# Optimization experiments

Measured on AMD Instinct MI355X. Metric: run time of the kernel, lower is better.

## Reference

```python
import jax, jax.numpy as jnp
import numpy as np

V, T, E, H, B, S = 50000, 45, 256, 512, 32, 256


def setup_inputs() -> dict:
    key = jax.random.key(0)
    ks = jax.random.split(key, 14)
    s = 0.05
    return dict(
        x=jax.random.randint(ks[0], (B, S), 0, V),
        tags=jax.random.randint(ks[1], (B, S), 0, T),
        mask=jnp.ones((B, S), dtype=bool),
        emb=jax.random.normal(ks[2], (V, E), jnp.float32),
        Wih_f=jax.random.normal(ks[3], (4 * H, E), jnp.float32) * s,
        Whh_f=jax.random.normal(ks[4], (4 * H, H), jnp.float32) * s,
        bih_f=jnp.zeros((4 * H,), jnp.float32),
        bhh_f=jnp.zeros((4 * H,), jnp.float32),
        Wih_b=jax.random.normal(ks[5], (4 * H, E), jnp.float32) * s,
        Whh_b=jax.random.normal(ks[6], (4 * H, H), jnp.float32) * s,
        bih_b=jnp.zeros((4 * H,), jnp.float32),
        bhh_b=jnp.zeros((4 * H,), jnp.float32),
        Wout=jax.random.normal(ks[7], (T, 2 * H), jnp.float32) * s,
        bout=jnp.zeros((T,), jnp.float32),
        start=jax.random.normal(ks[8], (T,), jnp.float32) * 0.1,
        end=jax.random.normal(ks[9], (T,), jnp.float32) * 0.1,
        trans=jax.random.normal(ks[10], (T, T), jnp.float32) * 0.1,
    )


def _lstm_dir(xp, Whh, reverse):
    # xp: [S, B, 4H] precomputed input projection + biases; gate order i,f,g,o (torch)
    Bn = xp.shape[1]
    Hn = Whh.shape[1]
    def step(carry, g_in):
        h, c = carry
        g = g_in + h @ Whh.T
        i, f, gg, o = jnp.split(g, 4, axis=-1)
        c = jax.nn.sigmoid(f) * c + jax.nn.sigmoid(i) * jnp.tanh(gg)
        h = jax.nn.sigmoid(o) * jnp.tanh(c)
        return (h, c), h
    init = (jnp.zeros((Bn, Hn), xp.dtype), jnp.zeros((Bn, Hn), xp.dtype))
    _, hs = jax.lax.scan(step, init, xp, reverse=reverse)
    return hs  # [S, B, H]


def _crf_nll(emissions, tags, mask, start, end, trans):
    # emissions: [B, S, T]; neg mean log-likelihood (torchcrf, reduction='mean')
    mf = mask.astype(emissions.dtype)
    em_tag = jnp.take_along_axis(emissions, tags[:, :, None], axis=2)[:, :, 0]  # [B,S]
    num = start[tags[:, 0]] + em_tag[:, 0]
    num = num + ((trans[tags[:, :-1], tags[:, 1:]] + em_tag[:, 1:]) * mf[:, 1:]).sum(1)
    seq_ends = mf.sum(1).astype(tags.dtype) - 1
    last_tags = jnp.take_along_axis(tags, seq_ends[:, None], axis=1)[:, 0]
    num = num + end[last_tags]
    def denom_step(alpha, inp):
        em_t, m_t = inp  # [B,T], [B]
        nxt = jax.nn.logsumexp(alpha[:, :, None] + trans[None, :, :] + em_t[:, None, :], axis=1)
        return jnp.where(m_t[:, None] > 0, nxt, alpha), None
    alpha0 = start[None, :] + emissions[:, 0]
    em_rest = emissions.transpose(1, 0, 2)[1:]  # [S-1, B, T]
    alpha, _ = jax.lax.scan(denom_step, alpha0, (em_rest, mf.T[1:]))
    logZ = jax.nn.logsumexp(alpha + end[None, :], axis=1)
    return -(num - logZ).mean()


def reference(x, tags, mask, emb, Wih_f, Whh_f, bih_f, bhh_f,
              Wih_b, Whh_b, bih_b, bhh_b, Wout, bout, start, end, trans):
    embeds = emb[x]                      # [B, S, E]
    xs = embeds.transpose(1, 0, 2)       # [S, B, E]
    xp_f = jnp.einsum('sbe,ge->sbg', xs, Wih_f) + bih_f + bhh_f
    hs_f = _lstm_dir(xp_f, Whh_f, False)
    xp_b = jnp.einsum('sbe,ge->sbg', xs, Wih_b) + bih_b + bhh_b
    hs_b = _lstm_dir(xp_b, Whh_b, True)
    hcat = jnp.concatenate([hs_f, hs_b], axis=-1)          # [S, B, 2H]
    emissions = jnp.einsum('sbh,th->sbt', hcat, Wout) + bout
    emissions = emissions.transpose(1, 0, 2)                # [B, S, T]
    return _crf_nll(emissions, tags, mask, start, end, trans)
```

## Files before the change

kernel.cpp:

```cpp
#include <hip/hip_runtime.h>
#include <stdint.h>

#define S_LEN 256
#define B_N 32
#define H_N 512
#define E_N 256
#define T_N 45
#define G4H 2048

typedef unsigned short u16;
typedef unsigned int u32;
typedef u16 u16x8 __attribute__((ext_vector_type(8)));
typedef u16 u16x4 __attribute__((ext_vector_type(4)));
typedef u32 u32x4 __attribute__((ext_vector_type(4)));
typedef __bf16 bf16x8 __attribute__((ext_vector_type(8)));
typedef float f32x4 __attribute__((ext_vector_type(4)));
typedef unsigned long long u64;

#define OFF_FLG   0ull
#define OFF_ATOK  256ull
#define OFF_WIHF  (OFF_ATOK + 4194304ull)
#define OFF_WIHB  (OFF_WIHF + 1048576ull)
#define OFF_WHHF  (OFF_WIHB + 1048576ull)
#define OFF_WHHB  (OFF_WHHF + 2097152ull)
#define OFF_WOUT  (OFF_WHHB + 2097152ull)
#define OFF_BSF   (OFF_WOUT + 98304ull)
#define OFF_BSB   (OFF_BSF + 8192ull)
#define OFF_XPF   (OFF_BSB + 8192ull)
#define OFF_XPB   (OFF_XPF + 33554432ull)
#define OFF_HSF   (OFF_XPB + 33554432ull)
#define OFF_HSB   (OFF_HSF + 8421376ull)
#define OFF_EM    (OFF_HSB + 8421376ull)
#define OFF_VAL   (OFF_EM + 1572864ull)

__device__ __forceinline__ u16 f2bf(float f) {
  union { float f; unsigned u; } v; v.f = f;
  unsigned r = v.u + 0x7FFFu + ((v.u >> 16) & 1u);
  return (u16)(r >> 16);
}
__device__ __forceinline__ float bf2f(u16 b) {
  union { unsigned u; float f; } v; v.u = ((unsigned)b) << 16;
  return v.f;
}
__device__ __forceinline__ bf16x8 ld8(const u16* p) {
  u16x8 v = *reinterpret_cast<const u16x8*>(p);
  return __builtin_bit_cast(bf16x8, v);
}
__device__ __forceinline__ void st_h8cc(u16* p, u16x4 v) {
  __hip_atomic_store(reinterpret_cast<u64*>(p), __builtin_bit_cast(u64, v),
                     __ATOMIC_RELAXED, __HIP_MEMORY_SCOPE_AGENT);
}
__device__ __forceinline__ u32x4 ld16cc(const u16* p) {
  u32x4 r;
  asm volatile("global_load_dwordx4 %0, %1, off sc0 sc1"
               : "=v"(r) : "v"(p) : "memory");
  return r;
}
__device__ __forceinline__ f32x4 mfma16(bf16x8 a, bf16x8 b, f32x4 c) {
  return __builtin_amdgcn_mfma_f32_16x16x32_bf16(a, b, c, 0, 0, 0);
}
__device__ __forceinline__ float sigm(float x) { return 1.f / (1.f + __expf(-x)); }
__device__ __forceinline__ float tanhf_(float x) {
  float ax = fabsf(x);
  float e = __expf(-2.f * ax);
  float t = 1.f - 2.f * e / (1.f + e);
  return (x < 0.f) ? -t : t;
}
__device__ __forceinline__ float wredmax(float v) {
  #pragma unroll
  for (int m = 1; m < 64; m <<= 1) v = fmaxf(v, __shfl_xor(v, m));
  return v;
}
__device__ __forceinline__ float wredsum(float v) {
  #pragma unroll
  for (int m = 1; m < 64; m <<= 1) v += __shfl_xor(v, m);
  return v;
}

__global__ void k_castA(const int* __restrict__ x, const float* __restrict__ emb,
                        u16* __restrict__ atok) {
  int idx = blockIdx.x * 256 + threadIdx.x;
  int t = idx >> 5;
  int e0 = (idx & 31) << 3;
  int s = t >> 5, b = t & 31;
  int xid = x[b * S_LEN + s];
  const float4* p = reinterpret_cast<const float4*>(emb + (size_t)xid * E_N + e0);
  float4 lo = p[0], hi = p[1];
  u16x8 o;
  o[0] = f2bf(lo.x); o[1] = f2bf(lo.y); o[2] = f2bf(lo.z); o[3] = f2bf(lo.w);
  o[4] = f2bf(hi.x); o[5] = f2bf(hi.y); o[6] = f2bf(hi.z); o[7] = f2bf(hi.w);
  *reinterpret_cast<u16x8*>(atok + (size_t)t * E_N + e0) = o;
}

__global__ void k_castW(const float* __restrict__ WihF, const float* __restrict__ WihB,
                        const float* __restrict__ WhhF, const float* __restrict__ WhhB,
                        const float* __restrict__ Wout,
                        const float* __restrict__ bihF, const float* __restrict__ bhhF,
                        const float* __restrict__ bihB, const float* __restrict__ bhhB,
                        u16* wihf, u16* wihb, u16* whhf, u16* whhb, u16* woutp,
                        float* bsf, float* bsb, u16* hsf, u16* hsb) {
  int i = blockIdx.x * 256 + threadIdx.x;
  if (i < 524288) { wihf[i] = f2bf(WihF[i]); return; }
  i -= 524288;
  if (i < 524288) { wihb[i] = f2bf(WihB[i]); return; }
  i -= 524288;
  if (i < 1048576) { whhf[i] = f2bf(WhhF[i]); return; }
  i -= 1048576;
  if (i < 1048576) { whhb[i] = f2bf(WhhB[i]); return; }
  i -= 1048576;
  if (i < 49152) {
    int n = i >> 10, k = i & 1023;
    woutp[i] = (n < T_N) ? f2bf(Wout[n * 1024 + k]) : (u16)0;
    return;
  }
  i -= 49152;
  if (i < 2048) { bsf[i] = bihF[i] + bhhF[i]; return; }
  i -= 2048;
  if (i < 2048) { bsb[i] = bihB[i] + bhhB[i]; return; }
  i -= 2048;
  if (i < 16384) { hsf[i] = 0; return; }
  i -= 16384;
  if (i < 16384) { hsb[(size_t)256 * 16384 + i] = 0; return; }
}

__global__ __launch_bounds__(256) void k_gemm_xp(
    const u16* __restrict__ atok, const u16* __restrict__ wihF, const u16* __restrict__ wihB,
    const float* __restrict__ bsF, const float* __restrict__ bsB,
    u16* __restrict__ xpF, u16* __restrict__ xpB) {
  int wid = blockIdx.x;
  int dir = wid >> 10, rem = wid & 1023;
  const int wave = threadIdx.x >> 6, lane = threadIdx.x & 63;
  const int lr = lane & 15, lh = lane >> 4;
  const int t0 = (rem >> 3) * 64;
  const int g0 = (rem & 7) * 256 + wave * 64;
  const u16* wih = dir ? wihB : wihF;
  const float* bs = dir ? bsB : bsF;
  u16* xp = dir ? xpB : xpF;
  f32x4 acc[4][4] = {};
  for (int kk = 0; kk < 8; ++kk) {
    int e = kk * 32 + lh * 8;
    bf16x8 a[4], bfr[4];
    #pragma unroll
    for (int mi = 0; mi < 4; ++mi) a[mi] = ld8(atok + (size_t)(t0 + 16 * mi + lr) * E_N + e);
    #pragma unroll
    for (int ni = 0; ni < 4; ++ni) bfr[ni] = ld8(wih + (size_t)(g0 + 16 * ni + lr) * E_N + e);
    #pragma unroll
    for (int mi = 0; mi < 4; ++mi)
      #pragma unroll
      for (int ni = 0; ni < 4; ++ni) acc[mi][ni] = mfma16(a[mi], bfr[ni], acc[mi][ni]);
  }
  #pragma unroll
  for (int ni = 0; ni < 4; ++ni) {
    int g = g0 + 16 * ni + lr;
    float bsv = bs[g];
    #pragma unroll
    for (int mi = 0; mi < 4; ++mi)
      #pragma unroll
      for (int r = 0; r < 4; ++r) {
        int t = t0 + 16 * mi + 4 * lh + r;
        xp[(size_t)t * G4H + g] = f2bf(acc[mi][ni][r] + bsv);
      }
  }
}

__global__ __launch_bounds__(128, 1) void k_lstm(
    const u16* __restrict__ whhF, const u16* __restrict__ whhB,
    const u16* __restrict__ xpF, const u16* __restrict__ xpB,
    u16* __restrict__ hsF, u16* __restrict__ hsB, int* flags) {
  const int dir = blockIdx.x >> 5;
  const int w = blockIdx.x & 31;
  const int nt = threadIdx.x >> 6;
  const int lane = threadIdx.x & 63;
  const int lr = lane & 15, lh = lane >> 4;
  const u16* whh = dir ? whhB : whhF;
  const u16* xp = dir ? xpB : xpF;
  u16* hs = dir ? hsB : hsF;
  int* flg = flags + dir * 32;

  bf16x8 A[4][16];
  #pragma unroll
  for (int mt = 0; mt < 4; ++mt) {
    const u16* base = whh + (size_t)(mt * 512 + 16 * w + lr) * H_N + lh * 8;
    #pragma unroll
    for (int kk = 0; kk < 16; ++kk) A[mt][kk] = ld8(base + kk * 32);
  }
  const int b = nt * 16 + lr;
  const int j0 = 16 * w + 4 * lh;
  const int fidx = lane & 31;
  float cst[4] = {0.f, 0.f, 0.f, 0.f};

  for (int t = 0; t < S_LEN; ++t) {
    const int s = dir ? (S_LEN - 1 - t) : t;
    const int slot_r = dir ? (s + 1) : s;
    const int slot_w = dir ? s : (s + 1);
    u16x4 xq[4];
    const u16* xpt = xp + ((size_t)(s * B_N + b)) * G4H + j0;
    #pragma unroll
    for (int mt = 0; mt < 4; ++mt) xq[mt] = *reinterpret_cast<const u16x4*>(xpt + mt * 512);

    const u16* hp = hs + ((size_t)slot_r * B_N + b) * H_N + lh * 8;
    u32x4 raw[16];
    #pragma unroll
    for (int kk = 0; kk < 16; ++kk) raw[kk] = ld16cc(hp + kk * 32);
    asm volatile("s_waitcnt vmcnt(0)" ::: "memory");
    __builtin_amdgcn_sched_barrier(0);
    u32 bad = 0;
    #pragma unroll
    for (int kk = 0; kk < 16; ++kk) {
      #pragma unroll
      for (int d = 0; d < 4; ++d) bad |= (raw[kk][d] == 0xFFFFFFFFu) ? 1u : 0u;
    }
    if (!__all(bad == 0)) {
      for (;;) {
        int f = __hip_atomic_load(&flg[fidx], __ATOMIC_RELAXED, __HIP_MEMORY_SCOPE_AGENT);
        if (__all(f >= t)) break;
        __builtin_amdgcn_s_sleep(1);
      }
      #pragma unroll
      for (int kk = 0; kk < 16; ++kk) raw[kk] = ld16cc(hp + kk * 32);
      asm volatile("s_waitcnt vmcnt(0)" ::: "memory");
      __builtin_amdgcn_sched_barrier(0);
    }

    f32x4 acc[4] = {};
    #pragma unroll
    for (int kk = 0; kk < 16; ++kk) {
      bf16x8 Bf = __builtin_bit_cast(bf16x8, raw[kk]);
      #pragma unroll
      for (int mt = 0; mt < 4; ++mt) acc[mt] = mfma16(A[mt][kk], Bf, acc[mt]);
    }
    u16x4 hv;
    #pragma unroll
    for (int r = 0; r < 4; ++r) {
      float gi = acc[0][r] + bf2f(xq[0][r]);
      float gf = acc[1][r] + bf2f(xq[1][r]);
      float gg = acc[2][r] + bf2f(xq[2][r]);
      float go = acc[3][r] + bf2f(xq[3][r]);
      float c = sigm(gf) * cst[r] + sigm(gi) * tanhf_(gg);
      cst[r] = c;
      hv[r] = f2bf(sigm(go) * tanhf_(c));
    }
    st_h8cc(hs + ((size_t)slot_w * B_N + b) * H_N + j0, hv);
    asm volatile("s_waitcnt vmcnt(0)" ::: "memory");
    __syncthreads();
    if (threadIdx.x == 0)
      __hip_atomic_store(&flg[w], t + 1, __ATOMIC_RELAXED, __HIP_MEMORY_SCOPE_AGENT);
  }
}

__global__ __launch_bounds__(256) void k_gemm_em(
    const u16* __restrict__ hsF, const u16* __restrict__ hsB,
    const u16* __restrict__ woutp, const float* __restrict__ bout, float* __restrict__ em) {
  const int wave = threadIdx.x >> 6, lane = threadIdx.x & 63;
  const int lr = lane & 15, lh = lane >> 4;
  const int t0 = blockIdx.x * 64 + wave * 16;
  f32x4 acc[3] = {};
  for (int kk = 0; kk < 32; ++kk) {
    int k = kk * 32 + lh * 8;
    int t = t0 + lr;
    int s = t >> 5, bt = t & 31;
    const u16* ap = (kk < 16) ? (hsF + ((size_t)(s + 1) * B_N + bt) * H_N + k)
                              : (hsB + ((size_t)s * B_N + bt) * H_N + (k - 512));
    bf16x8 a = ld8(ap);
    #pragma unroll
    for (int ni = 0; ni < 3; ++ni) {
      bf16x8 bb = ld8(woutp + (size_t)(16 * ni + lr) * 1024 + k);
      acc[ni] = mfma16(a, bb, acc[ni]);
    }
  }
  #pragma unroll
  for (int ni = 0; ni < 3; ++ni) {
    int tag = 16 * ni + lr;
    float bo = (tag < T_N) ? bout[tag] : 0.f;
    #pragma unroll
    for (int r = 0; r < 4; ++r) {
      int t = t0 + 4 * lh + r;
      em[(size_t)t * 48 + tag] = acc[ni][r] + bo;
    }
  }
}

__global__ __launch_bounds__(256) void k_crf(
    const float* __restrict__ em, const int* __restrict__ tags,
    const float* __restrict__ start, const float* __restrict__ endv,
    const float* __restrict__ trans, float* __restrict__ val) {
  __shared__ float tl[T_N * T_N];
  __shared__ float al[64];
  __shared__ float part[4][64];
  const int b = blockIdx.x;
  const int tid = threadIdx.x, wq = tid >> 6, lane = tid & 63;
  for (int i = tid; i < T_N * T_N; i += 256) tl[i] = trans[i];
  __syncthreads();
  float acur = (lane < T_N) ? (start[lane] + em[(size_t)b * 48 + lane]) : -1e30f;
  float shift = wredmax(acur);
  if (wq == 0) al[lane] = acur;
  __syncthreads();
  const int tbeg = wq * 12;
  const int tend = (tbeg + 12 < T_N) ? (tbeg + 12) : T_N;
  for (int s = 1; s < S_LEN; ++s) {
    float sm = 0.f;
    if (lane < T_N) {
      for (int t = tbeg; t < tend; ++t)
        sm += __expf(al[t] + tl[t * T_N + lane] - shift);
    }
    part[wq][lane] = sm;
    __syncthreads();
    float tot = part[0][lane] + part[1][lane] + part[2][lane] + part[3][lane];
    float anew = -1e30f;
    if (lane < T_N) anew = shift + __logf(tot) + em[((size_t)s * B_N + b) * 48 + lane];
    acur = anew;
    shift = wredmax(acur);
    __syncthreads();
    if (wq == 0) al[lane] = acur;
    __syncthreads();
  }
  float z = (lane < T_N) ? (acur + endv[lane]) : -1e30f;
  float m = wredmax(z);
  float sum = wredsum((lane < T_N) ? __expf(z - m) : 0.f);
  float logZ = m + __logf(sum);
  if (wq == 0) {
    float np = 0.f;
    #pragma unroll
    for (int q = 0; q < 4; ++q) {
      int s = 1 + lane * 4 + q;
      if (s < S_LEN) {
        int tp = tags[b * S_LEN + s - 1], tc = tags[b * S_LEN + s];
        np += tl[tp * T_N + tc] + em[((size_t)s * B_N + b) * 48 + tc];
      }
    }
    np = wredsum(np);
    if (lane == 0) {
      int tg0 = tags[b * S_LEN], tgL = tags[b * S_LEN + S_LEN - 1];
      float num = start[tg0] + em[(size_t)b * 48 + tg0] + np + endv[tgL];
      val[b] = num - logZ;
    }
  }
}

__global__ void k_final(const float* __restrict__ val, float* __restrict__ out) {
  int lane = threadIdx.x & 63;
  float v = (lane < B_N) ? val[lane] : 0.f;
  v = wredsum(v);
  if (threadIdx.x == 0) out[0] = -(v / (float)B_N);
}

extern "C" void kernel_launch(void* const* d_in, const int* in_sizes, int n_in,
                              void* d_out, int out_size, void* d_ws, size_t ws_size,
                              hipStream_t stream) {
  const int* x = (const int*)d_in[0];
  const int* tags = (const int*)d_in[1];
  const float* emb = (const float*)d_in[3];
  const float* WihF = (const float*)d_in[4];
  const float* WhhF = (const float*)d_in[5];
  const float* bihF = (const float*)d_in[6];
  const float* bhhF = (const float*)d_in[7];
  const float* WihB = (const float*)d_in[8];
  const float* WhhB = (const float*)d_in[9];
  const float* bihB = (const float*)d_in[10];
  const float* bhhB = (const float*)d_in[11];
  const float* Wout = (const float*)d_in[12];
  const float* bout = (const float*)d_in[13];
  const float* start = (const float*)d_in[14];
  const float* endv = (const float*)d_in[15];
  const float* trans = (const float*)d_in[16];
  float* out = (float*)d_out;
  char* ws = (char*)d_ws;

  u16* atok = (u16*)(ws + OFF_ATOK);
  u16* wihf = (u16*)(ws + OFF_WIHF);
  u16* wihb = (u16*)(ws + OFF_WIHB);
  u16* whhf = (u16*)(ws + OFF_WHHF);
  u16* whhb = (u16*)(ws + OFF_WHHB);
  u16* woutp = (u16*)(ws + OFF_WOUT);
  float* bsf = (float*)(ws + OFF_BSF);
  float* bsb = (float*)(ws + OFF_BSB);
  u16* xpf = (u16*)(ws + OFF_XPF);
  u16* xpb = (u16*)(ws + OFF_XPB);
  u16* hsf = (u16*)(ws + OFF_HSF);
  u16* hsb = (u16*)(ws + OFF_HSB);
  float* emis = (float*)(ws + OFF_EM);
  float* val = (float*)(ws + OFF_VAL);

  hipMemsetAsync(ws + OFF_FLG, 0, 256, stream);
  hipMemsetAsync(ws + OFF_HSF + 32768ull, 0xFF, 8388608ull, stream);
  hipMemsetAsync(ws + OFF_HSB, 0xFF, 8388608ull, stream);
  k_castA<<<1024, 256, 0, stream>>>(x, emb, atok);
  k_castW<<<12624, 256, 0, stream>>>(WihF, WihB, WhhF, WhhB, Wout, bihF, bhhF, bihB, bhhB,
                                     wihf, wihb, whhf, whhb, woutp, bsf, bsb, hsf, hsb);
  k_gemm_xp<<<2048, 256, 0, stream>>>(atok, wihf, wihb, bsf, bsb, xpf, xpb);
  k_lstm<<<64, 128, 0, stream>>>(whhf, whhb, xpf, xpb, hsf, hsb, (int*)(ws + OFF_FLG));
  k_gemm_em<<<128, 256, 0, stream>>>(hsf, hsb, woutp, bout, emis);
  k_crf<<<32, 256, 0, stream>>>(emis, tags, start, endv, trans, val);
  k_final<<<1, 64, 0, stream>>>(val, out);
}
```

Baseline: 1.527 ms.

## Switch LSTM to per-wave flag sync and single-wave shuffle-based CRF

The LSTM recurrence drops its speculative sentinel-value check (0xFF-filled h buffers plus a reload on a miss). Instead, each wave polls 64 per-wave flags before loading h, and the block-wide __syncthreads is gone because each wave publishes its own flag. This also removes the two 8MB memsets of the h buffers. The CRF forward pass moves from four waves with shared-memory partial sums and three barriers per step to one wave using shuffles and three independent accumulators. The trade-off is that every step now pays a flag-polling round trip even when data is already ready.

```diff
diff --git a/kernel.cpp b/kernel.cpp
--- a/kernel.cpp
+++ b/kernel.cpp
@@ -18,7 +18,7 @@
 typedef unsigned long long u64;
 
 #define OFF_FLG   0ull
-#define OFF_ATOK  256ull
+#define OFF_ATOK  1024ull
 #define OFF_WIHF  (OFF_ATOK + 4194304ull)
 #define OFF_WIHB  (OFF_WIHF + 1048576ull)
 #define OFF_WHHF  (OFF_WIHB + 1048576ull)
@@ -175,7 +175,8 @@
   const u16* whh = dir ? whhB : whhF;
   const u16* xp = dir ? xpB : xpF;
   u16* hs = dir ? hsB : hsF;
-  int* flg = flags + dir * 32;
+  int* flg = flags + dir * 64;
+  const int myf = w * 2 + nt;
 
   bf16x8 A[4][16];
   #pragma unroll
@@ -186,7 +187,6 @@
   }
   const int b = nt * 16 + lr;
   const int j0 = 16 * w + 4 * lh;
-  const int fidx = lane & 31;
   float cst[4] = {0.f, 0.f, 0.f, 0.f};
 
   for (int t = 0; t < S_LEN; ++t) {
@@ -198,29 +198,20 @@
     #pragma unroll
     for (int mt = 0; mt < 4; ++mt) xq[mt] = *reinterpret_cast<const u16x4*>(xpt + mt * 512);
 
+    if (t > 0) {
+      for (;;) {
+        int f = __hip_atomic_load(&flg[lane], __ATOMIC_RELAXED, __HIP_MEMORY_SCOPE_AGENT);
+        if (__all(f >= t)) break;
+        __builtin_amdgcn_s_sleep(1);
+      }
+    }
+
     const u16* hp = hs + ((size_t)slot_r * B_N + b) * H_N + lh * 8;
     u32x4 raw[16];
     #pragma unroll
     for (int kk = 0; kk < 16; ++kk) raw[kk] = ld16cc(hp + kk * 32);
     asm volatile("s_waitcnt vmcnt(0)" ::: "memory");
     __builtin_amdgcn_sched_barrier(0);
-    u32 bad = 0;
-    #pragma unroll
-    for (int kk = 0; kk < 16; ++kk) {
-      #pragma unroll
-      for (int d = 0; d < 4; ++d) bad |= (raw[kk][d] == 0xFFFFFFFFu) ? 1u : 0u;
-    }
-    if (!__all(bad == 0)) {
-      for (;;) {
-        int f = __hip_atomic_load(&flg[fidx], __ATOMIC_RELAXED, __HIP_MEMORY_SCOPE_AGENT);
-        if (__all(f >= t)) break;
-        __builtin_amdgcn_s_sleep(1);
-      }
-      #pragma unroll
-      for (int kk = 0; kk < 16; ++kk) raw[kk] = ld16cc(hp + kk * 32);
-      asm volatile("s_waitcnt vmcnt(0)" ::: "memory");
-      __builtin_amdgcn_sched_barrier(0);
-    }
 
     f32x4 acc[4] = {};
     #pragma unroll
@@ -242,9 +233,8 @@
     }
     st_h8cc(hs + ((size_t)slot_w * B_N + b) * H_N + j0, hv);
     asm volatile("s_waitcnt vmcnt(0)" ::: "memory");
-    __syncthreads();
-    if (threadIdx.x == 0)
-      __hip_atomic_store(&flg[w], t + 1, __ATOMIC_RELAXED, __HIP_MEMORY_SCOPE_AGENT);
+    if (lane == 0)
+      __hip_atomic_store(&flg[myf], t + 1, __ATOMIC_RELAXED, __HIP_MEMORY_SCOPE_AGENT);
   }
 }
 
@@ -280,60 +270,47 @@
   }
 }
 
-__global__ __launch_bounds__(256) void k_crf(
+__global__ __launch_bounds__(64) void k_crf(
     const float* __restrict__ em, const int* __restrict__ tags,
     const float* __restrict__ start, const float* __restrict__ endv,
     const float* __restrict__ trans, float* __restrict__ val) {
-  __shared__ float tl[T_N * T_N];
-  __shared__ float al[64];
-  __shared__ float part[4][64];
+  __shared__ float tl[T_N * T_N + 32];
   const int b = blockIdx.x;
-  const int tid = threadIdx.x, wq = tid >> 6, lane = tid & 63;
-  for (int i = tid; i < T_N * T_N; i += 256) tl[i] = trans[i];
+  const int lane = threadIdx.x;
+  for (int i = lane; i < T_N * T_N + 32; i += 64)
+    tl[i] = (i < T_N * T_N) ? trans[i] : 0.f;
   __syncthreads();
   float acur = (lane < T_N) ? (start[lane] + em[(size_t)b * 48 + lane]) : -1e30f;
-  float shift = wredmax(acur);
-  if (wq == 0) al[lane] = acur;
-  __syncthreads();
-  const int tbeg = wq * 12;
-  const int tend = (tbeg + 12 < T_N) ? (tbeg + 12) : T_N;
   for (int s = 1; s < S_LEN; ++s) {
-    float sm = 0.f;
-    if (lane < T_N) {
-      for (int t = tbeg; t < tend; ++t)
-        sm += __expf(al[t] + tl[t * T_N + lane] - shift);
-    }
-    part[wq][lane] = sm;
-    __syncthreads();
-    float tot = part[0][lane] + part[1][lane] + part[2][lane] + part[3][lane];
-    float anew = -1e30f;
-    if (lane < T_N) anew = shift + __logf(tot) + em[((size_t)s * B_N + b) * 48 + lane];
-    acur = anew;
-    shift = wredmax(acur);
-    __syncthreads();
-    if (wq == 0) al[lane] = acur;
-    __syncthreads();
+    float shift = wredmax(acur);
+    float emv = (lane < 48) ? em[((size_t)s * B_N + b) * 48 + lane] : 0.f;
+    float s0 = 0.f, s1 = 0.f, s2 = 0.f;
+    #pragma unroll
+    for (int t = 0; t < T_N; t += 3) {
+      s0 += __expf(__shfl(acur, t)     + tl[t * T_N + lane]       - shift);
+      s1 += __expf(__shfl(acur, t + 1) + tl[(t + 1) * T_N + lane] - shift);
+      s2 += __expf(__shfl(acur, t + 2) + tl[(t + 2) * T_N + lane] - shift);
+    }
+    acur = (lane < T_N) ? (shift + __logf(s0 + s1 + s2) + emv) : -1e30f;
   }
   float z = (lane < T_N) ? (acur + endv[lane]) : -1e30f;
   float m = wredmax(z);
   float sum = wredsum((lane < T_N) ? __expf(z - m) : 0.f);
   float logZ = m + __logf(sum);
-  if (wq == 0) {
-    float np = 0.f;
-    #pragma unroll
-    for (int q = 0; q < 4; ++q) {
-      int s = 1 + lane * 4 + q;
-      if (s < S_LEN) {
-        int tp = tags[b * S_LEN + s - 1], tc = tags[b * S_LEN + s];
-        np += tl[tp * T_N + tc] + em[((size_t)s * B_N + b) * 48 + tc];
-      }
-    }
-    np = wredsum(np);
-    if (lane == 0) {
-      int tg0 = tags[b * S_LEN], tgL = tags[b * S_LEN + S_LEN - 1];
-      float num = start[tg0] + em[(size_t)b * 48 + tg0] + np + endv[tgL];
-      val[b] = num - logZ;
-    }
+  float np = 0.f;
+  #pragma unroll
+  for (int q = 0; q < 4; ++q) {
+    int s = 1 + lane * 4 + q;
+    if (s < S_LEN) {
+      int tp = tags[b * S_LEN + s - 1], tc = tags[b * S_LEN + s];
+      np += tl[tp * T_N + tc] + em[((size_t)s * B_N + b) * 48 + tc];
+    }
+  }
+  np = wredsum(np);
+  if (lane == 0) {
+    int tg0 = tags[b * S_LEN], tgL = tags[b * S_LEN + S_LEN - 1];
+    float num = start[tg0] + em[(size_t)b * 48 + tg0] + np + endv[tgL];
+    val[b] = num - logZ;
   }
 }
 
@@ -381,15 +358,13 @@
   float* emis = (float*)(ws + OFF_EM);
   float* val = (float*)(ws + OFF_VAL);
 
-  hipMemsetAsync(ws + OFF_FLG, 0, 256, stream);
-  hipMemsetAsync(ws + OFF_HSF + 32768ull, 0xFF, 8388608ull, stream);
-  hipMemsetAsync(ws + OFF_HSB, 0xFF, 8388608ull, stream);
+  hipMemsetAsync(ws + OFF_FLG, 0, 1024, stream);
   k_castA<<<1024, 256, 0, stream>>>(x, emb, atok);
   k_castW<<<12624, 256, 0, stream>>>(WihF, WihB, WhhF, WhhB, Wout, bihF, bhhF, bihB, bhhB,
                                      wihf, wihb, whhf, whhb, woutp, bsf, bsb, hsf, hsb);
   k_gemm_xp<<<2048, 256, 0, stream>>>(atok, wihf, wihb, bsf, bsb, xpf, xpb);
   k_lstm<<<64, 128, 0, stream>>>(whhf, whhb, xpf, xpb, hsf, hsb, (int*)(ws + OFF_FLG));
   k_gemm_em<<<128, 256, 0, stream>>>(hsf, hsb, woutp, bout, emis);
-  k_crf<<<32, 256, 0, stream>>>(emis, tags, start, endv, trans, val);
+  k_crf<<<32, 64, 0, stream>>>(emis, tags, start, endv, trans, val);
   k_final<<<1, 64, 0, stream>>>(val, out);
 }
```

After: 1.740 ms. +13.9%, slower.
